# Kernel tuning notes

Measured on AMD Instinct MI355X. Metric: run time of the kernel, lower is better.

Reference implementation:

```python
import jax, jax.numpy as jnp
import numpy as np

NUM_HEADS = 16
NUM_KV_HEADS = 4
HEAD_DIM = 128
SCALE = 0.08838834764831845  # 1/sqrt(128)
BATCH = 4
SEQLEN = 1024
TOTAL = BATCH * SEQLEN


def setup_inputs() -> dict:
    key = jax.random.key(0)
    kq, kk, kv = jax.random.split(key, 3)
    q = jax.random.normal(kq, (TOTAL, NUM_HEADS, HEAD_DIM), dtype=jnp.float32)
    k = jax.random.normal(kk, (TOTAL, NUM_KV_HEADS, HEAD_DIM), dtype=jnp.float32)
    v = jax.random.normal(kv, (TOTAL, NUM_KV_HEADS, HEAD_DIM), dtype=jnp.float32)
    cu = jnp.arange(BATCH + 1, dtype=jnp.int32) * SEQLEN  # [0,1024,2048,3072,4096]
    return {"q": q, "k": k, "v": v, "cu_seqlens_q": cu, "cu_seqlens_k": cu}


def reference(q, k, v, cu_seqlens_q, cu_seqlens_k):
    # Prefill varlen causal attention (block_tables=None, empty kv cache).
    # Equal-length segments -> reshape packed tokens to [B, S, H, D].
    B = cu_seqlens_q.shape[0] - 1
    S = q.shape[0] // B
    H, Dh = q.shape[1], q.shape[2]
    Hkv = k.shape[1]
    g = H // Hkv  # GQA group size

    qb = q.reshape(B, S, H, Dh)
    # repeat_interleave kv heads to match query heads
    kb = jnp.repeat(k.reshape(B, S, Hkv, Dh), g, axis=2)  # [B,S,H,Dh]
    vb = jnp.repeat(v.reshape(B, S, Hkv, Dh), g, axis=2)

    scores = jnp.einsum('bqhd,bkhd->bhqk', qb, kb) * SCALE  # [B,H,S,S]
    causal = jnp.tril(jnp.ones((S, S), dtype=bool))
    scores = jnp.where(causal, scores, jnp.finfo(scores.dtype).min)
    probs = jax.nn.softmax(scores, axis=-1)
    o = jnp.einsum('bhqk,bkhd->bqhd', probs, vb)  # [B,S,H,Dh]
    return o.reshape(B * S, H, Dh)
```

## Files before the change

### kernel.cpp

```cpp
#include <hip/hip_runtime.h>
#include <hip/hip_bf16.h>
#include <cstddef>

#define NH 16
#define NKV 4
#define HD 128
#define SEQ 1024
#define SCALE_F 0.08838834764831845f
#define LOG2E 1.44269504088896f

typedef __attribute__((ext_vector_type(8))) short short8;
typedef __attribute__((ext_vector_type(4))) float floatx4;
typedef __attribute__((ext_vector_type(2))) unsigned int uintx2;

union F8 { short8 v; unsigned short u[8]; };

__device__ __forceinline__ unsigned short f2bf(float f) {
  unsigned int u = __float_as_uint(f);
  u += 0x7FFFu + ((u >> 16) & 1u);
  return (unsigned short)(u >> 16);
}

__device__ __forceinline__ unsigned int pkbf(float a, float b) {
  union { __hip_bfloat162 h; unsigned int u; } c;
  c.h = __float22bfloat162_rn(float2{a, b});
  return c.u;
}

__device__ __forceinline__ void glds16(const void* g, void* l) {
  __builtin_amdgcn_global_load_lds(
      (const __attribute__((address_space(1))) unsigned int*)g,
      (__attribute__((address_space(3))) unsigned int*)l, 16, 0, 0);
}

__global__ __launch_bounds__(256) void prepass(const float* __restrict__ kg,
                                               const float* __restrict__ vg,
                                               unsigned short* __restrict__ Ktg,
                                               unsigned short* __restrict__ Vtg) {
  __shared__ float Vl[32 * 132];
  const int tid = threadIdx.x;
  const int bid = blockIdx.x;
  if (bid < 512) {
    const int bkvh = bid >> 5, tile = bid & 31;
    const int b = bkvh >> 2, kvh = bkvh & 3;
    const int kpos = tid >> 3;
    const int d8base = (tid & 7) * 2;
    const size_t tok = (size_t)b * SEQ + tile * 32 + kpos;
    const float* src = kg + (tok * NKV + kvh) * HD + d8base * 8;
    unsigned short* dstT = Ktg + (size_t)bid * 4096;
#pragma unroll
    for (int i = 0; i < 2; ++i) {
      floatx4 a = ((const floatx4*)src)[0];
      floatx4 c = ((const floatx4*)src)[1];
      F8 t;
#pragma unroll
      for (int j = 0; j < 4; ++j) { t.u[j] = f2bf(a[j]); t.u[4 + j] = f2bf(c[j]); }
      const int blk = kpos * 16 + ((d8base + i) ^ (kpos & 15));
      *(short8*)(dstT + blk * 8) = t.v;
      src += 8;
    }
  } else {
    const int bb2 = bid - 512;
    const int bkvh = bb2 >> 5, tile = bb2 & 31;
    const int b = bkvh >> 2, kvh = bkvh & 3;
    const int r = tid >> 3;
    const int c16 = (tid & 7) * 16;
    const size_t tok = (size_t)b * SEQ + tile * 32 + r;
    const float* src = vg + (tok * NKV + kvh) * HD + c16;
#pragma unroll
    for (int j = 0; j < 4; ++j)
      *(floatx4*)&Vl[r * 132 + c16 + j * 4] = ((const floatx4*)src)[j];
    __syncthreads();
    unsigned short* dstT = Vtg + (size_t)bb2 * 4096;
#pragma unroll
    for (int i = 0; i < 2; ++i) {
      const int s = tid * 2 + i;
      const int dt = s >> 6;
      const int ln = s & 63;
      const int qd = ln >> 4;
      const int cl = ln & 15;
      F8 t;
#pragma unroll
      for (int j = 0; j < 8; ++j)
        t.u[j] = f2bf(Vl[(qd * 8 + j) * 132 + dt * 16 + cl]);
      *(short8*)(dstT + s * 8) = t.v;
    }
  }
}

__global__ __launch_bounds__(128, 3)
void fa_fwd4(const float* __restrict__ qg, const unsigned short* __restrict__ Ktg,
             const unsigned short* __restrict__ Vtg, float* __restrict__ og) {
  __shared__ __align__(16) unsigned short Kb[2][4096];
  __shared__ __align__(16) unsigned int Pbuf[2][512];

  const int tid = threadIdx.x;
  const int w = tid >> 6;
  const int lane = tid & 63;
  const int col = lane & 15;
  const int quad = lane >> 4;

  const int idx = blockIdx.x;
  const int qt = 31 - (idx >> 6);
  const int bh = idx & 63;
  const int h = bh & 15;
  const int b = bh >> 4;
  const int kvh = h >> 2;
  const int seg = b * SEQ;
  const int q0 = qt * 32;
  const size_t tbase = (size_t)((b * NKV + kvh) * 32) * 8192;

  F8 qf[2][4];
#pragma unroll
  for (int nt = 0; nt < 2; ++nt) {
    const float* qp =
        qg + ((size_t)(seg + q0 + nt * 16 + col) * NH + h) * HD + quad * 8;
#pragma unroll
    for (int ks = 0; ks < 4; ++ks) {
      floatx4 a = ((const floatx4*)(qp + ks * 32))[0];
      floatx4 c = ((const floatx4*)(qp + ks * 32))[1];
#pragma unroll
      for (int j = 0; j < 4; ++j) {
        qf[nt][ks].u[j] = f2bf(a[j] * (SCALE_F * LOG2E));
        qf[nt][ks].u[4 + j] = f2bf(c[j] * (SCALE_F * LOG2E));
      }
    }
  }

  floatx4 acc[2][8];
#pragma unroll
  for (int nt = 0; nt < 2; ++nt)
#pragma unroll
    for (int dt = 0; dt < 8; ++dt) acc[nt][dt] = (floatx4){0.f, 0.f, 0.f, 0.f};
  float lsum[2] = {0.f, 0.f};

  char* lk = (char*)&Kb[w][0];
  if (w <= qt) {
    const char* gk = (const char*)Ktg + tbase + (size_t)w * 8192 + lane * 16;
#pragma unroll
    for (int o = 0; o < 8192; o += 1024) glds16(gk + o, lk + o);
  }

  for (int p = w; p <= qt; p += 2) {
    __builtin_amdgcn_s_waitcnt(0x0f70);
    __builtin_amdgcn_sched_barrier(0);
    F8 vf[8];
    const char* vsrc = (const char*)Vtg + tbase + (size_t)p * 8192 + lane * 16;
#pragma unroll
    for (int dt = 0; dt < 8; ++dt) vf[dt].v = *(const short8*)(vsrc + dt * 1024);
    floatx4 st[2][2];
#pragma unroll
    for (int nt = 0; nt < 2; ++nt)
#pragma unroll
      for (int hh = 0; hh < 2; ++hh) st[nt][hh] = (floatx4){0.f, 0.f, 0.f, 0.f};
#pragma unroll
    for (int hh = 0; hh < 2; ++hh)
#pragma unroll
      for (int ks = 0; ks < 4; ++ks) {
        F8 kf;
        kf.v = *(const short8*)&Kb[w][hh * 2048 +
                                      (col * 16 + ((ks * 4 + quad) ^ col)) * 8];
        st[0][hh] = __builtin_amdgcn_mfma_f32_16x16x32_bf16(
            kf.v, qf[0][ks].v, st[0][hh], 0, 0, 0);
        st[1][hh] = __builtin_amdgcn_mfma_f32_16x16x32_bf16(
            kf.v, qf[1][ks].v, st[1][hh], 0, 0, 0);
      }
    __builtin_amdgcn_sched_barrier(0);
    if (p + 2 <= qt) {
      const char* gk =
          (const char*)Ktg + tbase + (size_t)(p + 2) * 8192 + lane * 16;
#pragma unroll
      for (int o = 0; o < 8192; o += 1024) glds16(gk + o, lk + o);
    }
    __builtin_amdgcn_sched_barrier(0);
    const bool diag = (p == qt);
#pragma unroll
    for (int nt = 0; nt < 2; ++nt)
#pragma unroll
      for (int hh = 0; hh < 2; ++hh) {
        float pr[4];
#pragma unroll
        for (int r = 0; r < 4; ++r) {
          pr[r] = exp2f(st[nt][hh][r]);
          if (diag && (p * 32 + hh * 16 + quad * 4 + r > q0 + nt * 16 + col))
            pr[r] = 0.f;
        }
        lsum[nt] += (pr[0] + pr[1]) + (pr[2] + pr[3]);
        const int bbi = hh * 2 + (quad >> 1);
        unsigned int* pw = &Pbuf[w][(nt * 16 + col) * 16 +
                                    ((bbi ^ (col & 3)) << 2) + ((quad & 1) << 1)];
        *(uintx2*)pw = (uintx2){pkbf(pr[0], pr[1]), pkbf(pr[2], pr[3])};
      }
    F8 pb[2];
#pragma unroll
    for (int nt = 0; nt < 2; ++nt)
      pb[nt].v = *(const short8*)&Pbuf[w][(nt * 16 + col) * 16 +
                                          ((quad ^ (col & 3)) << 2)];
#pragma unroll
    for (int dt = 0; dt < 8; ++dt)
#pragma unroll
      for (int nt = 0; nt < 2; ++nt)
        acc[nt][dt] = __builtin_amdgcn_mfma_f32_16x16x32_bf16(
            vf[dt].v, pb[nt].v, acc[nt][dt], 0, 0, 0);
  }

  __syncthreads();
  float* cb = (float*)&Kb[0][0];
  float* lb = (float*)&Pbuf[0][0];
  if (w == 1) {
#pragma unroll
    for (int nt = 0; nt < 2; ++nt)
#pragma unroll
      for (int dt = 0; dt < 8; ++dt)
        *(floatx4*)&cb[((nt * 8 + dt) * 64 + lane) * 4] = acc[nt][dt];
    lb[lane] = lsum[0];
    lb[64 + lane] = lsum[1];
  }
  __syncthreads();
  if (w == 0) {
#pragma unroll
    for (int nt = 0; nt < 2; ++nt) {
      float l = lsum[nt] + lb[nt * 64 + lane];
      l += __shfl_xor(l, 16);
      l += __shfl_xor(l, 32);
      const float inv = 1.0f / l;
      float* op = og + ((size_t)(seg + q0 + nt * 16 + col) * NH + h) * HD +
                  quad * 4;
#pragma unroll
      for (int dt = 0; dt < 8; ++dt) {
        floatx4 o = acc[nt][dt] + *(const floatx4*)&cb[((nt * 8 + dt) * 64 + lane) * 4];
        o[0] *= inv; o[1] *= inv; o[2] *= inv; o[3] *= inv;
        *(floatx4*)(op + dt * 16) = o;
      }
    }
  }
}

#define KST 136
#define VST 40
#define PST 40

__global__ __launch_bounds__(256, 2)
void fa_fwd(const float* __restrict__ qg, const float* __restrict__ kg,
            const float* __restrict__ vg, float* __restrict__ og) {
  __shared__ unsigned short Klds[32 * KST];
  __shared__ unsigned short Vt[HD * VST];
  __shared__ unsigned short Pl[4][32 * PST];

  const int tid = threadIdx.x;
  const int wave = tid >> 6;
  const int lane = tid & 63;
  const int col = lane & 15;
  const int quad = lane >> 4;

  const int idx = blockIdx.x;
  const int raw = idx & 7;
  const int qt = (idx & 256) ? raw : 7 - raw;
  const int bh = idx >> 3;
  const int h = bh & 15;
  const int b = bh >> 4;
  const int kvh = h >> 2;
  const int seg = b * SEQ;
  const int wq0 = qt * 128 + wave * 32;

  F8 qf[2][4];
#pragma unroll
  for (int mt = 0; mt < 2; ++mt) {
    const size_t qrow = (size_t)(seg + wq0 + mt * 16 + col);
    const float* qp = qg + (qrow * NH + h) * HD + quad * 8;
#pragma unroll
    for (int ks = 0; ks < 4; ++ks) {
      const floatx4* p4 = (const floatx4*)(qp + ks * 32);
      floatx4 a = p4[0], c = p4[1];
#pragma unroll
      for (int j = 0; j < 4; ++j) {
        qf[mt][ks].u[j] = f2bf(a[j] * SCALE_F);
        qf[mt][ks].u[4 + j] = f2bf(c[j] * SCALE_F);
      }
    }
  }

  floatx4 acc[2][8];
#pragma unroll
  for (int mt = 0; mt < 2; ++mt)
#pragma unroll
    for (int dt = 0; dt < 8; ++dt)
      acc[mt][dt] = (floatx4){0.f, 0.f, 0.f, 0.f};
  float lsum[2][4];
#pragma unroll
  for (int mt = 0; mt < 2; ++mt)
#pragma unroll
    for (int r = 0; r < 4; ++r) lsum[mt][r] = 0.f;

  const int nkt = 4 * (qt + 1);
  const int sr = tid >> 3;
  const int sc = (tid & 7) * 16;

  for (int kt = 0; kt < nkt; ++kt) {
    const int kbase = kt * 32;
    __syncthreads();
    {
      const size_t tok = (size_t)(seg + kbase + sr);
      const floatx4* kp4 = (const floatx4*)(kg + (tok * NKV + kvh) * HD + sc);
      floatx4 kv0 = kp4[0], kv1 = kp4[1], kv2 = kp4[2], kv3 = kp4[3];
      float kf32[16] = {kv0[0],kv0[1],kv0[2],kv0[3], kv1[0],kv1[1],kv1[2],kv1[3],
                        kv2[0],kv2[1],kv2[2],kv2[3], kv3[0],kv3[1],kv3[2],kv3[3]};
      unsigned int* dst = (unsigned int*)&Klds[sr * KST + sc];
#pragma unroll
      for (int j = 0; j < 8; ++j)
        dst[j] = (unsigned int)f2bf(kf32[2 * j]) | ((unsigned int)f2bf(kf32[2 * j + 1]) << 16);
      const floatx4* vp4 = (const floatx4*)(vg + (tok * NKV + kvh) * HD + sc);
      floatx4 vv0 = vp4[0], vv1 = vp4[1], vv2 = vp4[2], vv3 = vp4[3];
      unsigned short vb[16] = {
        f2bf(vv0[0]),f2bf(vv0[1]),f2bf(vv0[2]),f2bf(vv0[3]),
        f2bf(vv1[0]),f2bf(vv1[1]),f2bf(vv1[2]),f2bf(vv1[3]),
        f2bf(vv2[0]),f2bf(vv2[1]),f2bf(vv2[2]),f2bf(vv2[3]),
        f2bf(vv3[0]),f2bf(vv3[1]),f2bf(vv3[2]),f2bf(vv3[3])};
#pragma unroll
      for (int s = 0; s < 16; ++s) {
        int j = (s + tid) & 15;
        Vt[(sc + j) * VST + sr] = vb[j];
      }
    }
    __syncthreads();

    if (kbase > wq0 + 31) continue;

    F8 kf[4][2];
#pragma unroll
    for (int ks = 0; ks < 4; ++ks)
#pragma unroll
      for (int nt = 0; nt < 2; ++nt)
        kf[ks][nt].v = *(const short8*)&Klds[(nt * 16 + col) * KST + ks * 32 + quad * 8];

#pragma unroll
    for (int mt = 0; mt < 2; ++mt) {
      floatx4 s0 = {0.f, 0.f, 0.f, 0.f}, s1 = {0.f, 0.f, 0.f, 0.f};
#pragma unroll
      for (int ks = 0; ks < 4; ++ks) {
        s0 = __builtin_amdgcn_mfma_f32_16x16x32_bf16(qf[mt][ks].v, kf[ks][0].v, s0, 0, 0, 0);
        s1 = __builtin_amdgcn_mfma_f32_16x16x32_bf16(qf[mt][ks].v, kf[ks][1].v, s1, 0, 0, 0);
      }
      const int q0 = wq0 + mt * 16 + quad * 4;
      const bool diag = (kbase + 31 > wq0 + mt * 16);
      unsigned short* pw = &Pl[wave][(mt * 16 + quad * 4) * PST];
#pragma unroll
      for (int r = 0; r < 4; ++r) {
        float p0 = __expf(s0[r]);
        float p1 = __expf(s1[r]);
        if (diag) {
          p0 = (kbase + col > q0 + r) ? 0.f : p0;
          p1 = (kbase + 16 + col > q0 + r) ? 0.f : p1;
        }
        lsum[mt][r] += p0 + p1;
        pw[r * PST + col] = f2bf(p0);
        pw[r * PST + 16 + col] = f2bf(p1);
      }
    }
    F8 pa[2];
#pragma unroll
    for (int mt = 0; mt < 2; ++mt)
      pa[mt].v = *(const short8*)&Pl[wave][(mt * 16 + col) * PST + quad * 8];
#pragma unroll
    for (int dt = 0; dt < 8; ++dt) {
      F8 vb;
      vb.v = *(const short8*)&Vt[(dt * 16 + col) * VST + quad * 8];
#pragma unroll
      for (int mt = 0; mt < 2; ++mt)
        acc[mt][dt] = __builtin_amdgcn_mfma_f32_16x16x32_bf16(pa[mt].v, vb.v, acc[mt][dt], 0, 0, 0);
    }
  }

#pragma unroll
  for (int mt = 0; mt < 2; ++mt) {
#pragma unroll
    for (int r = 0; r < 4; ++r) {
      float l = lsum[mt][r];
      l += __shfl_xor(l, 1);
      l += __shfl_xor(l, 2);
      l += __shfl_xor(l, 4);
      l += __shfl_xor(l, 8);
      const float inv = 1.0f / l;
      const int qi = wq0 + mt * 16 + quad * 4 + r;
      float* op = og + ((size_t)(seg + qi) * NH + h) * HD;
#pragma unroll
      for (int dt = 0; dt < 8; ++dt)
        op[dt * 16 + col] = acc[mt][dt][r] * inv;
    }
  }
}

extern "C" void kernel_launch(void* const* d_in, const int* in_sizes, int n_in,
                              void* d_out, int out_size, void* d_ws, size_t ws_size,
                              hipStream_t stream) {
  const float* q = (const float*)d_in[0];
  const float* k = (const float*)d_in[1];
  const float* v = (const float*)d_in[2];
  float* out = (float*)d_out;
  if (ws_size >= (size_t)(8 * 1024 * 1024)) {
    unsigned short* Ktg = (unsigned short*)d_ws;
    unsigned short* Vtg = Ktg + 2097152;
    hipLaunchKernelGGL(prepass, dim3(1024), dim3(256), 0, stream, k, v, Ktg, Vtg);
    hipLaunchKernelGGL(fa_fwd4, dim3(2048), dim3(128), 0, stream, q, Ktg, Vtg, out);
  } else {
    hipLaunchKernelGGL(fa_fwd, dim3(512), dim3(256), 0, stream, q, k, v, out);
  }
}
```

Measured before the change: 143.0 us.

## Load K fragments directly from global in MFMA order, drop LDS K staging

The prepass now writes K tiles in the exact per-lane MFMA fragment order, so the attention kernel reads K straight from global/L2 into registers instead of staging it through double-buffered LDS with async global_load_lds. The output combine is split per nt and uses a smaller dedicated buffer, cutting shared memory so occupancy can go from 3 to 4 blocks per CU. The cost is that the explicit K prefetch overlap is lost and the K loads now depend on cache hits with no manual pipelining.

```diff
diff --git a/kernel.cpp b/kernel.cpp
--- a/kernel.cpp
+++ b/kernel.cpp
@@ -25,12 +25,6 @@
   union { __hip_bfloat162 h; unsigned int u; } c;
   c.h = __float22bfloat162_rn(float2{a, b});
   return c.u;
-}
-
-__device__ __forceinline__ void glds16(const void* g, void* l) {
-  __builtin_amdgcn_global_load_lds(
-      (const __attribute__((address_space(1))) unsigned int*)g,
-      (__attribute__((address_space(3))) unsigned int*)l, 16, 0, 0);
 }
 
 __global__ __launch_bounds__(256) void prepass(const float* __restrict__ kg,
@@ -48,6 +42,7 @@
     const size_t tok = (size_t)b * SEQ + tile * 32 + kpos;
     const float* src = kg + (tok * NKV + kvh) * HD + d8base * 8;
     unsigned short* dstT = Ktg + (size_t)bid * 4096;
+    const int hh = kpos >> 4, col = kpos & 15;
 #pragma unroll
     for (int i = 0; i < 2; ++i) {
       floatx4 a = ((const floatx4*)src)[0];
@@ -55,8 +50,9 @@
       F8 t;
 #pragma unroll
       for (int j = 0; j < 4; ++j) { t.u[j] = f2bf(a[j]); t.u[4 + j] = f2bf(c[j]); }
-      const int blk = kpos * 16 + ((d8base + i) ^ (kpos & 15));
-      *(short8*)(dstT + blk * 8) = t.v;
+      const int d8 = d8base + i;
+      const int slot = ((hh * 4 + (d8 >> 2)) * 64) + ((d8 & 3) * 16) + col;
+      *(short8*)(dstT + slot * 8) = t.v;
       src += 8;
     }
   } else {
@@ -88,11 +84,12 @@
   }
 }
 
-__global__ __launch_bounds__(128, 3)
-void fa_fwd4(const float* __restrict__ qg, const unsigned short* __restrict__ Ktg,
+__global__ __launch_bounds__(128, 4)
+void fa_fwd5(const float* __restrict__ qg, const unsigned short* __restrict__ Ktg,
              const unsigned short* __restrict__ Vtg, float* __restrict__ og) {
-  __shared__ __align__(16) unsigned short Kb[2][4096];
   __shared__ __align__(16) unsigned int Pbuf[2][512];
+  __shared__ __align__(16) float Comb[2048];
+  __shared__ float Lcomb[128];
 
   const int tid = threadIdx.x;
   const int w = tid >> 6;
@@ -108,7 +105,10 @@
   const int kvh = h >> 2;
   const int seg = b * SEQ;
   const int q0 = qt * 32;
-  const size_t tbase = (size_t)((b * NKV + kvh) * 32) * 8192;
+  const char* kvbase =
+      (const char*)Ktg + (size_t)((b * NKV + kvh) * 32) * 8192 + lane * 16;
+  const char* vvbase =
+      (const char*)Vtg + (size_t)((b * NKV + kvh) * 32) * 8192 + lane * 16;
 
   F8 qf[2][4];
 #pragma unroll
@@ -134,20 +134,9 @@
     for (int dt = 0; dt < 8; ++dt) acc[nt][dt] = (floatx4){0.f, 0.f, 0.f, 0.f};
   float lsum[2] = {0.f, 0.f};
 
-  char* lk = (char*)&Kb[w][0];
-  if (w <= qt) {
-    const char* gk = (const char*)Ktg + tbase + (size_t)w * 8192 + lane * 16;
-#pragma unroll
-    for (int o = 0; o < 8192; o += 1024) glds16(gk + o, lk + o);
-  }
-
   for (int p = w; p <= qt; p += 2) {
-    __builtin_amdgcn_s_waitcnt(0x0f70);
-    __builtin_amdgcn_sched_barrier(0);
-    F8 vf[8];
-    const char* vsrc = (const char*)Vtg + tbase + (size_t)p * 8192 + lane * 16;
-#pragma unroll
-    for (int dt = 0; dt < 8; ++dt) vf[dt].v = *(const short8*)(vsrc + dt * 1024);
+    const char* kp = kvbase + (size_t)p * 8192;
+    const char* vp = vvbase + (size_t)p * 8192;
     floatx4 st[2][2];
 #pragma unroll
     for (int nt = 0; nt < 2; ++nt)
@@ -158,21 +147,16 @@
 #pragma unroll
       for (int ks = 0; ks < 4; ++ks) {
         F8 kf;
-        kf.v = *(const short8*)&Kb[w][hh * 2048 +
-                                      (col * 16 + ((ks * 4 + quad) ^ col)) * 8];
+        kf.v = *(const short8*)(kp + (hh * 4 + ks) * 1024);
         st[0][hh] = __builtin_amdgcn_mfma_f32_16x16x32_bf16(
             kf.v, qf[0][ks].v, st[0][hh], 0, 0, 0);
         st[1][hh] = __builtin_amdgcn_mfma_f32_16x16x32_bf16(
             kf.v, qf[1][ks].v, st[1][hh], 0, 0, 0);
       }
-    __builtin_amdgcn_sched_barrier(0);
-    if (p + 2 <= qt) {
-      const char* gk =
-          (const char*)Ktg + tbase + (size_t)(p + 2) * 8192 + lane * 16;
-#pragma unroll
-      for (int o = 0; o < 8192; o += 1024) glds16(gk + o, lk + o);
-    }
-    __builtin_amdgcn_sched_barrier(0);
+    F8 vf[8];
+#pragma unroll
+    for (int dt = 0; dt < 8; ++dt)
+      vf[dt].v = *(const short8*)(vp + dt * 1024);
     const bool diag = (p == qt);
 #pragma unroll
     for (int nt = 0; nt < 2; ++nt)
@@ -204,23 +188,21 @@
             vf[dt].v, pb[nt].v, acc[nt][dt], 0, 0, 0);
   }
 
-  __syncthreads();
-  float* cb = (float*)&Kb[0][0];
-  float* lb = (float*)&Pbuf[0][0];
   if (w == 1) {
-#pragma unroll
-    for (int nt = 0; nt < 2; ++nt)
+    Lcomb[lane] = lsum[0];
+    Lcomb[64 + lane] = lsum[1];
+  }
+#pragma unroll
+  for (int nt = 0; nt < 2; ++nt) {
+    __syncthreads();
+    if (w == 1) {
 #pragma unroll
       for (int dt = 0; dt < 8; ++dt)
-        *(floatx4*)&cb[((nt * 8 + dt) * 64 + lane) * 4] = acc[nt][dt];
-    lb[lane] = lsum[0];
-    lb[64 + lane] = lsum[1];
-  }
-  __syncthreads();
-  if (w == 0) {
-#pragma unroll
-    for (int nt = 0; nt < 2; ++nt) {
-      float l = lsum[nt] + lb[nt * 64 + lane];
+        *(floatx4*)&Comb[(dt * 64 + lane) * 4] = acc[nt][dt];
+    }
+    __syncthreads();
+    if (w == 0) {
+      float l = lsum[nt] + Lcomb[nt * 64 + lane];
       l += __shfl_xor(l, 16);
       l += __shfl_xor(l, 32);
       const float inv = 1.0f / l;
@@ -228,7 +210,7 @@
                   quad * 4;
 #pragma unroll
       for (int dt = 0; dt < 8; ++dt) {
-        floatx4 o = acc[nt][dt] + *(const floatx4*)&cb[((nt * 8 + dt) * 64 + lane) * 4];
+        floatx4 o = acc[nt][dt] + *(const floatx4*)&Comb[(dt * 64 + lane) * 4];
         o[0] *= inv; o[1] *= inv; o[2] *= inv; o[3] *= inv;
         *(floatx4*)(op + dt * 16) = o;
       }
@@ -401,7 +383,7 @@
     unsigned short* Ktg = (unsigned short*)d_ws;
     unsigned short* Vtg = Ktg + 2097152;
     hipLaunchKernelGGL(prepass, dim3(1024), dim3(256), 0, stream, k, v, Ktg, Vtg);
-    hipLaunchKernelGGL(fa_fwd4, dim3(2048), dim3(128), 0, stream, q, Ktg, Vtg, out);
+    hipLaunchKernelGGL(fa_fwd5, dim3(2048), dim3(128), 0, stream, q, Ktg, Vtg, out);
   } else {
     hipLaunchKernelGGL(fa_fwd, dim3(512), dim3(256), 0, stream, q, k, v, out);
   }
```

After: 182.2 us. 1.27x slower.
